# Kernel optimization log

Hardware: AMD Instinct MI355X
Metric: run time of the kernel (lower is better)

The kernel has to match this reference:

```python
import jax, jax.numpy as jnp
import numpy as np

LN_EPS = 1e-5

def _layernorm(x, g, b):
    mu = jnp.mean(x, axis=-1, keepdims=True)
    var = jnp.mean((x - mu) ** 2, axis=-1, keepdims=True)
    return (x - mu) * jax.lax.rsqrt(var + LN_EPS) * g + b

def _linear_init(k, fan_in, fan_out):
    s = 1.0 / np.sqrt(fan_in)
    kw, kb = jax.random.split(k)
    W = jax.random.uniform(kw, (fan_in, fan_out), jnp.float32, -s, s)
    b = jax.random.uniform(kb, (fan_out,), jnp.float32, -s, s)
    return W, b

def setup_inputs() -> dict:
    key = jax.random.key(0)
    ks = jax.random.split(key, 8)
    B, C, H, W = 4, 256, 64, 64
    Cout = 256
    N = H * W
    E = 16 * N
    x = jax.random.normal(ks[0], (B, C, H, W), jnp.float32)
    edge_index = jax.random.randint(ks[1], (2, E), 0, N)
    W1, b1 = _linear_init(ks[2], C, 1024)
    W2, b2 = _linear_init(ks[3], 1024, 512)
    W3, b3 = _linear_init(ks[4], 512, Cout)
    return {
        'x': x, 'edge_index': edge_index,
        'W1': W1, 'b1': b1, 'g1': jnp.ones(1024, jnp.float32), 'be1': jnp.zeros(1024, jnp.float32),
        'W2': W2, 'b2': b2, 'g2': jnp.ones(512, jnp.float32), 'be2': jnp.zeros(512, jnp.float32),
        'W3': W3, 'b3': b3, 'g_out': jnp.ones(Cout, jnp.float32), 'b_out': jnp.zeros(Cout, jnp.float32),
    }

def reference(x, edge_index, W1, b1, g1, be1, W2, b2, g2, be2, W3, b3, g_out, b_out):
    B, C, H, Wd = x.shape
    N = H * Wd
    # [B, N, C] node features (pixels as nodes)
    x_flat = x.reshape(B, C, N).transpose(0, 2, 1)
    # Dense adjacency from edge list (duplicates sum, same as sparse->to_dense).
    # Identical for every batch item, so build once and broadcast through einsum.
    A = jnp.zeros((N, N), x.dtype).at[edge_index[0], edge_index[1]].add(1.0)
    A = A + jnp.eye(N, dtype=x.dtype)  # self-loops
    deg = jnp.sum(A, axis=-1)
    d_inv_sqrt = jnp.where(deg > 0, jax.lax.rsqrt(deg), 0.0)
    A_norm = d_inv_sqrt[:, None] * A * d_inv_sqrt[None, :]
    # message passing: [N,N] @ [B,N,C] -> [B,N,C]
    h = jnp.einsum('mn,bnc->bmc', A_norm, x_flat)
    h = _layernorm(jax.nn.relu(h @ W1 + b1), g1, be1)
    h = _layernorm(jax.nn.relu(h @ W2 + b2), g2, be2)
    h = h @ W3 + b3
    h = _layernorm(h, g_out, b_out)
    return h.transpose(0, 2, 1).reshape(B, -1, H, Wd)
```

## Files before the change

kernel.cpp:

```cpp
#include <hip/hip_runtime.h>

typedef __attribute__((ext_vector_type(8))) short short8_t;
typedef __attribute__((ext_vector_type(4))) float f32x4;

#define AS1 __attribute__((address_space(1)))
#define AS3 __attribute__((address_space(3)))

static_assert(sizeof(short8_t) == 16, "short8_t must be 16B");

__device__ __forceinline__ short f2bf(float f) {
  union { float f; unsigned u; } v; v.f = f;
  unsigned r = (v.u + 0x7FFFu + ((v.u >> 16) & 1u)) >> 16;
  return (short)r;
}
__device__ __forceinline__ float bf2f(short s) {
  union { unsigned u; float f; } v; v.u = ((unsigned)(unsigned short)s) << 16;
  return v.f;
}

__global__ __launch_bounds__(256) void count_deg(const int* __restrict__ ei,
                                                 int* __restrict__ deg, int E) {
  int e = blockIdx.x * 256 + threadIdx.x;
  if (e < E) atomicAdd(&deg[ei[e]], 1);
}

__global__ __launch_bounds__(1024) void scan_deg(const int* __restrict__ deg,
                                                 int* __restrict__ rp,
                                                 float* __restrict__ dis) {
  __shared__ int part[1024];
  const int t = threadIdx.x;
  int4 v = ((const int4*)deg)[t];
  const int s = v.x + v.y + v.z + v.w;
  part[t] = s;
  __syncthreads();
  for (int off = 1; off < 1024; off <<= 1) {
    int mine = part[t];
    int add = (t >= off) ? part[t - off] : 0;
    __syncthreads();
    part[t] = mine + add;
    __syncthreads();
  }
  const int excl = part[t] - s;
  const int b4 = t * 4;
  rp[b4 + 0] = excl;
  rp[b4 + 1] = excl + v.x;
  rp[b4 + 2] = excl + v.x + v.y;
  rp[b4 + 3] = excl + v.x + v.y + v.z;
  if (t == 1023) rp[4096] = part[1023];
  dis[b4 + 0] = rsqrtf((float)(v.x + 1));
  dis[b4 + 1] = rsqrtf((float)(v.y + 1));
  dis[b4 + 2] = rsqrtf((float)(v.z + 1));
  dis[b4 + 3] = rsqrtf((float)(v.w + 1));
}

__global__ __launch_bounds__(256) void prep(
    const int* __restrict__ ei, const int* __restrict__ rp, int* __restrict__ fil,
    int* __restrict__ cols, int E,
    const float* __restrict__ x, const float* __restrict__ dis, short* __restrict__ xs,
    const float* __restrict__ W1, const float* __restrict__ W2, const float* __restrict__ W3,
    const float* __restrict__ g1, const float* __restrict__ be1,
    const float* __restrict__ g2, const float* __restrict__ be2,
    short* __restrict__ w1t, short* __restrict__ w2t, short* __restrict__ w3t,
    float* __restrict__ cs2, float* __restrict__ ct2,
    float* __restrict__ cs3, float* __restrict__ ct3) {
  __shared__ float tile[32][33];
  const int tx = threadIdx.x, ty = threadIdx.y;
  const int bid = blockIdx.x;
  if (bid < 256) {
    const int e = bid * 256 + ty * 32 + tx;
    if (e < E) {
      const int r = ei[e], c = ei[E + e];
      const int p = atomicAdd(&fil[r], 1);
      cols[rp[r] + p] = c;
    }
    return;
  }
  if (bid < 256 + 4096) {
    const int id = bid - 256;
    const int b = id >> 10;
    const int n0 = ((id & 1023) >> 3) * 32;
    const int c0 = (id & 7) * 32;
    const float* xb = x + (long)b * (256 * 4096);
#pragma unroll
    for (int i = 0; i < 32; i += 8)
      tile[ty + i][tx] = xb[(long)(c0 + ty + i) * 4096 + n0 + tx];
    __syncthreads();
#pragma unroll
    for (int i = 0; i < 32; i += 8) {
      const int n = n0 + ty + i;
      xs[(long)n * 1024 + b * 256 + c0 + tx] = f2bf(tile[tx][ty + i] * dis[n]);
    }
    return;
  }
  int id = bid - 4352;
  const float *Wf, *g = nullptr, *be = nullptr;
  float *cs = nullptr, *ctp = nullptr;
  short* Wt;
  int K, N, k0, n0;
  if (id < 256)      { Wf = W1; Wt = w1t; K = 256;  N = 1024; k0 = (id & 7) * 32;  n0 = (id >> 3) * 32; }
  else if (id < 768) { id -= 256; Wf = W2; Wt = w2t; K = 1024; N = 512; k0 = (id & 31) * 32; n0 = (id >> 5) * 32;
                       g = g1; be = be1; cs = cs2; ctp = ct2; }
  else               { id -= 768; Wf = W3; Wt = w3t; K = 512;  N = 256; k0 = (id & 15) * 32; n0 = (id >> 4) * 32;
                       g = g2; be = be2; cs = cs3; ctp = ct3; }
  float csp = 0.f, ctv = 0.f;
#pragma unroll
  for (int i = 0; i < 32; i += 8) {
    const int k = k0 + ty + i;
    const float wv = Wf[(long)k * N + n0 + tx];
    const float gk = g ? g[k] : 1.0f;
    tile[ty + i][tx] = gk * wv;
    csp += gk * wv;
    if (be) ctv += be[k] * wv;
  }
  __syncthreads();
#pragma unroll
  for (int i = 0; i < 32; i += 8)
    Wt[(long)(n0 + ty + i) * K + k0 + tx] = f2bf(tile[tx][ty + i]);
  if (cs) {
    atomicAdd(&cs[n0 + tx], csp);
    atomicAdd(&ctp[n0 + tx], ctv);
  }
}

__global__ __launch_bounds__(256) void gather_mp(const short* __restrict__ xs,
                                                 const float* __restrict__ dis,
                                                 const int* __restrict__ rp,
                                                 const int* __restrict__ cols,
                                                 short* __restrict__ h0) {
  __shared__ int sc[256];
  const int m = blockIdx.x;
  const int t = threadIdx.x;
  short4 v0 = ((const short4*)(xs + (long)m * 1024))[t];
  float a0 = bf2f(v0.x), a1 = bf2f(v0.y), a2 = bf2f(v0.z), a3 = bf2f(v0.w);
  const int s = rp[m], e = rp[m + 1];
  for (int base = s; base < e; base += 256) {
    const int cnt = min(256, e - base);
    __syncthreads();
    if (t < cnt) sc[t] = cols[base + t];
    __syncthreads();
    for (int j = 0; j < cnt; ++j) {
      const int n = sc[j];
      short4 v = ((const short4*)(xs + (long)n * 1024))[t];
      a0 += bf2f(v.x); a1 += bf2f(v.y); a2 += bf2f(v.z); a3 += bf2f(v.w);
    }
  }
  const float d = dis[m];
  short4 o;
  o.x = f2bf(a0 * d); o.y = f2bf(a1 * d); o.z = f2bf(a2 * d); o.w = f2bf(a3 * d);
  const int b = t >> 6, c4 = t & 63;
  ((short4*)(h0 + (((long)b << 12) + m) * 256))[c4] = o;
}

template <bool LNIN, bool RELU>
__global__ __launch_bounds__(256, 2) void gemm_ln(
    const short* __restrict__ A, const short* __restrict__ Bt,
    const float* __restrict__ bias, const float* __restrict__ cs,
    const float* __restrict__ ct, const float* __restrict__ statsIn,
    float* __restrict__ statsOut, short* __restrict__ out,
    int M, int N, int K) {
  __shared__ __align__(16) short As[2][128 * 32];
  __shared__ __align__(16) short Bs[2][128 * 32];
  const int tid = threadIdx.x;
  const int lane = tid & 63;
  const int wave = tid >> 6;
  const int wm = wave >> 1, wn = wave & 1;
  const int m0 = blockIdx.x * 128, n0 = blockIdx.y * 128;

  f32x4 acc[4][4] = {};

  const int srow = wave * 32 + (lane >> 2);
  const int scol = (lane & 3) * 8;
  const short* ag = A + (long)(m0 + srow) * K + scol;
  const short* bg = Bt + (long)(n0 + srow) * K + scol;
  const int ldst = (wave * 32) * 32;
  const int fr = lane & 15;
  const int kc = (lane >> 4) * 8;
  const int NT = K >> 5;

#define STAGE(T, BUF)                                                                        \
  do {                                                                                       \
    const short* a_ = ag + (T) * 32;                                                         \
    const short* b_ = bg + (T) * 32;                                                         \
    __builtin_amdgcn_global_load_lds((const AS1 void*)a_, (AS3 void*)(&As[BUF][ldst]), 16, 0, 0); \
    __builtin_amdgcn_global_load_lds((const AS1 void*)(a_ + 16 * K), (AS3 void*)(&As[BUF][ldst + 512]), 16, 0, 0); \
    __builtin_amdgcn_global_load_lds((const AS1 void*)b_, (AS3 void*)(&Bs[BUF][ldst]), 16, 0, 0); \
    __builtin_amdgcn_global_load_lds((const AS1 void*)(b_ + 16 * K), (AS3 void*)(&Bs[BUF][ldst + 512]), 16, 0, 0); \
  } while (0)

  STAGE(0, 0);
  __syncthreads();
  int cur = 0;
  for (int t = 0; t < NT; ++t) {
    if (t + 1 < NT) STAGE(t + 1, cur ^ 1);
    short8_t af[4], bf[4];
#pragma unroll
    for (int i = 0; i < 4; ++i)
      af[i] = *(const short8_t*)&As[cur][(wm * 64 + i * 16 + fr) * 32 + kc];
#pragma unroll
    for (int i = 0; i < 4; ++i)
      bf[i] = *(const short8_t*)&Bs[cur][(wn * 64 + i * 16 + fr) * 32 + kc];
#pragma unroll
    for (int mi = 0; mi < 4; ++mi)
#pragma unroll
      for (int ni = 0; ni < 4; ++ni)
        acc[mi][ni] = __builtin_amdgcn_mfma_f32_16x16x32_bf16(af[mi], bf[ni],
                                                              acc[mi][ni], 0, 0, 0);
    __syncthreads();
    cur ^= 1;
  }
#undef STAGE

  const int rq = (lane >> 4) * 4;
  const float invK = 1.0f / (float)K;
  float bv[4], csv[4], ctv[4];
#pragma unroll
  for (int ni = 0; ni < 4; ++ni) {
    const int col = n0 + wn * 64 + ni * 16 + fr;
    bv[ni] = bias[col];
    if (LNIN) { csv[ni] = cs[col]; ctv[ni] = ct[col]; }
  }
#pragma unroll
  for (int mi = 0; mi < 4; ++mi) {
    float r1[4], rmu[4];
    if (LNIN) {
#pragma unroll
      for (int r = 0; r < 4; ++r) {
        const int row = m0 + wm * 64 + mi * 16 + rq + r;
        const float s = statsIn[row * 2];
        const float q = statsIn[row * 2 + 1];
        const float mu = s * invK;
        const float var = fmaxf(q * invK - mu * mu, 0.0f);
        const float rr = rsqrtf(var + 1e-5f);
        r1[r] = rr; rmu[r] = rr * mu;
      }
    }
    float sv[4] = {0, 0, 0, 0}, qv[4] = {0, 0, 0, 0};
#pragma unroll
    for (int ni = 0; ni < 4; ++ni) {
      const int col = n0 + wn * 64 + ni * 16 + fr;
#pragma unroll
      for (int r = 0; r < 4; ++r) {
        const int row = m0 + wm * 64 + mi * 16 + rq + r;
        float v = acc[mi][ni][r];
        if (LNIN) v = r1[r] * v - rmu[r] * csv[ni] + ctv[ni] + bv[ni];
        else      v = v + bv[ni];
        if (RELU) v = fmaxf(v, 0.0f);
        out[(long)row * N + col] = f2bf(v);
        sv[r] += v; qv[r] += v * v;
      }
    }
#pragma unroll
    for (int r = 0; r < 4; ++r) {
      float s = sv[r], q = qv[r];
#pragma unroll
      for (int off = 1; off < 16; off <<= 1) {
        s += __shfl_xor(s, off);
        q += __shfl_xor(q, off);
      }
      if (fr == 0) {
        const int row = m0 + wm * 64 + mi * 16 + rq + r;
        atomicAdd(&statsOut[row * 2], s);
        atomicAdd(&statsOut[row * 2 + 1], q);
      }
    }
  }
}

__global__ __launch_bounds__(256) void ln_tr_out(const short* __restrict__ t3,
                                                 const float* __restrict__ stats,
                                                 const float* __restrict__ g,
                                                 const float* __restrict__ be,
                                                 float* __restrict__ out) {
  __shared__ short tile[64][66];
  const int tx = threadIdx.x;
  const int ty = threadIdx.y;
  const int n0 = blockIdx.x * 64;
  const int c0 = blockIdx.y * 64;
  const int b = blockIdx.z;
  const long rbase = ((long)b << 12) + n0;
#pragma unroll
  for (int i = ty; i < 64; i += 4)
    tile[i][tx] = t3[(rbase + i) * 256 + c0 + tx];
  const float s = stats[(rbase + tx) * 2];
  const float q = stats[(rbase + tx) * 2 + 1];
  const float mu = s * (1.0f / 256.0f);
  const float var = fmaxf(q * (1.0f / 256.0f) - mu * mu, 0.0f);
  const float inv = rsqrtf(var + 1e-5f);
  __syncthreads();
  float* ob = out + ((long)b << 20) + n0 + tx;
#pragma unroll
  for (int i = ty; i < 64; i += 4) {
    const int c = c0 + i;
    ob[(long)c * 4096] = (bf2f(tile[tx][i]) - mu) * inv * g[c] + be[c];
  }
}

extern "C" void kernel_launch(void* const* d_in, const int* in_sizes, int n_in,
                              void* d_out, int out_size, void* d_ws, size_t ws_size,
                              hipStream_t stream) {
  (void)n_in; (void)out_size; (void)ws_size;
  const float* x   = (const float*)d_in[0];
  const int*   ei  = (const int*)d_in[1];
  const float* W1  = (const float*)d_in[2];
  const float* b1  = (const float*)d_in[3];
  const float* g1  = (const float*)d_in[4];
  const float* be1 = (const float*)d_in[5];
  const float* W2  = (const float*)d_in[6];
  const float* b2  = (const float*)d_in[7];
  const float* g2  = (const float*)d_in[8];
  const float* be2 = (const float*)d_in[9];
  const float* W3  = (const float*)d_in[10];
  const float* b3  = (const float*)d_in[11];
  const float* go  = (const float*)d_in[12];
  const float* bo  = (const float*)d_in[13];
  float* out = (float*)d_out;
  const int E = in_sizes[1] / 2;

  char* w = (char*)d_ws;
  int*   deg    = (int*)(w + 0);
  int*   fil    = (int*)(w + (16 << 10));
  float* stats1 = (float*)(w + (32 << 10));
  float* stats2 = (float*)(w + (160 << 10));
  float* stats3 = (float*)(w + (288 << 10));
  float* cs2    = (float*)(w + (416 << 10));
  float* ct2    = (float*)(w + (418 << 10));
  float* cs3    = (float*)(w + (420 << 10));
  float* ct3    = (float*)(w + (421 << 10));
  int*   rp   = (int*)(w + (424 << 10));
  float* dis  = (float*)(w + (444 << 10));
  int*   cols = (int*)(w + (460 << 10));
  short* w1t  = (short*)(w + (720 << 10));
  short* w2t  = (short*)(w + (1240 << 10));
  short* w3t  = (short*)(w + (2264 << 10));
  short* xs   = (short*)(w + (3ull << 20));
  short* h0   = (short*)(w + (11ull << 20));
  short* t1   = (short*)(w + (19ull << 20));
  short* t2   = (short*)(w + (51ull << 20));
  short* t3   = (short*)(w + (67ull << 20));

  hipMemsetAsync(d_ws, 0, 422 << 10, stream);
  count_deg<<<256, 256, 0, stream>>>(ei, deg, E);
  scan_deg<<<1, 1024, 0, stream>>>(deg, rp, dis);
  prep<<<5248, dim3(32, 8), 0, stream>>>(ei, rp, fil, cols, E, x, dis, xs,
                                         W1, W2, W3, g1, be1, g2, be2,
                                         w1t, w2t, w3t, cs2, ct2, cs3, ct3);
  gather_mp<<<4096, 256, 0, stream>>>(xs, dis, rp, cols, h0);
  gemm_ln<false, true><<<dim3(128, 8), 256, 0, stream>>>(
      h0, w1t, b1, nullptr, nullptr, nullptr, stats1, t1, 16384, 1024, 256);
  gemm_ln<true, true><<<dim3(128, 4), 256, 0, stream>>>(
      t1, w2t, b2, cs2, ct2, stats1, stats2, t2, 16384, 512, 1024);
  gemm_ln<true, false><<<dim3(128, 2), 256, 0, stream>>>(
      t2, w3t, b3, cs3, ct3, stats2, stats3, t3, 16384, 256, 512);
  ln_tr_out<<<dim3(64, 4, 4), dim3(64, 4), 0, stream>>>(t3, stats3, go, bo, out);
}
```

Before: 147.7 us.

## Triple-buffer GEMM LDS pipeline and unroll gather loop by four

```diff
diff --git a/kernel.cpp b/kernel.cpp
--- a/kernel.cpp
+++ b/kernel.cpp
@@ -138,7 +138,19 @@
     __syncthreads();
     if (t < cnt) sc[t] = cols[base + t];
     __syncthreads();
-    for (int j = 0; j < cnt; ++j) {
+    int j = 0;
+    for (; j + 4 <= cnt; j += 4) {
+      const int n0 = sc[j], n1 = sc[j + 1], n2 = sc[j + 2], n3 = sc[j + 3];
+      short4 w0 = ((const short4*)(xs + (long)n0 * 1024))[t];
+      short4 w1 = ((const short4*)(xs + (long)n1 * 1024))[t];
+      short4 w2 = ((const short4*)(xs + (long)n2 * 1024))[t];
+      short4 w3 = ((const short4*)(xs + (long)n3 * 1024))[t];
+      a0 += bf2f(w0.x) + bf2f(w1.x) + bf2f(w2.x) + bf2f(w3.x);
+      a1 += bf2f(w0.y) + bf2f(w1.y) + bf2f(w2.y) + bf2f(w3.y);
+      a2 += bf2f(w0.z) + bf2f(w1.z) + bf2f(w2.z) + bf2f(w3.z);
+      a3 += bf2f(w0.w) + bf2f(w1.w) + bf2f(w2.w) + bf2f(w3.w);
+    }
+    for (; j < cnt; ++j) {
       const int n = sc[j];
       short4 v = ((const short4*)(xs + (long)n * 1024))[t];
       a0 += bf2f(v.x); a1 += bf2f(v.y); a2 += bf2f(v.z); a3 += bf2f(v.w);
@@ -158,8 +170,8 @@
     const float* __restrict__ ct, const float* __restrict__ statsIn,
     float* __restrict__ statsOut, short* __restrict__ out,
     int M, int N, int K) {
-  __shared__ __align__(16) short As[2][128 * 32];
-  __shared__ __align__(16) short Bs[2][128 * 32];
+  __shared__ __align__(16) short As[3][128 * 32];
+  __shared__ __align__(16) short Bs[3][128 * 32];
   const int tid = threadIdx.x;
   const int lane = tid & 63;
   const int wave = tid >> 6;
@@ -187,28 +199,41 @@
     __builtin_amdgcn_global_load_lds((const AS1 void*)(b_ + 16 * K), (AS3 void*)(&Bs[BUF][ldst + 512]), 16, 0, 0); \
   } while (0)
 
+#define COMPUTE(RB)                                                                          \
+  do {                                                                                       \
+    short8_t af[4], bf[4];                                                                   \
+    _Pragma("unroll")                                                                        \
+    for (int i = 0; i < 4; ++i)                                                              \
+      af[i] = *(const short8_t*)&As[RB][(wm * 64 + i * 16 + fr) * 32 + kc];                  \
+    _Pragma("unroll")                                                                        \
+    for (int i = 0; i < 4; ++i)                                                              \
+      bf[i] = *(const short8_t*)&Bs[RB][(wn * 64 + i * 16 + fr) * 32 + kc];                  \
+    _Pragma("unroll")                                                                        \
+    for (int mi = 0; mi < 4; ++mi)                                                           \
+      _Pragma("unroll")                                                                      \
+      for (int ni = 0; ni < 4; ++ni)                                                         \
+        acc[mi][ni] = __builtin_amdgcn_mfma_f32_16x16x32_bf16(af[mi], bf[ni],                \
+                                                              acc[mi][ni], 0, 0, 0);         \
+  } while (0)
+
   STAGE(0, 0);
-  __syncthreads();
-  int cur = 0;
-  for (int t = 0; t < NT; ++t) {
-    if (t + 1 < NT) STAGE(t + 1, cur ^ 1);
-    short8_t af[4], bf[4];
-#pragma unroll
-    for (int i = 0; i < 4; ++i)
-      af[i] = *(const short8_t*)&As[cur][(wm * 64 + i * 16 + fr) * 32 + kc];
-#pragma unroll
-    for (int i = 0; i < 4; ++i)
-      bf[i] = *(const short8_t*)&Bs[cur][(wn * 64 + i * 16 + fr) * 32 + kc];
-#pragma unroll
-    for (int mi = 0; mi < 4; ++mi)
-#pragma unroll
-      for (int ni = 0; ni < 4; ++ni)
-        acc[mi][ni] = __builtin_amdgcn_mfma_f32_16x16x32_bf16(af[mi], bf[ni],
-                                                              acc[mi][ni], 0, 0, 0);
-    __syncthreads();
-    cur ^= 1;
-  }
+  STAGE(1, 1);
+  int rb = 0;
+  for (int t = 0; t < NT - 1; ++t) {
+    asm volatile("s_waitcnt vmcnt(4)" ::: "memory");
+    __builtin_amdgcn_s_barrier();
+    __builtin_amdgcn_sched_barrier(0);
+    int wb = rb + 2; if (wb >= 3) wb -= 3;
+    if (t + 2 < NT) STAGE(t + 2, wb);
+    COMPUTE(rb);
+    rb = (rb == 2) ? 0 : rb + 1;
+  }
+  asm volatile("s_waitcnt vmcnt(0)" ::: "memory");
+  __builtin_amdgcn_s_barrier();
+  __builtin_amdgcn_sched_barrier(0);
+  COMPUTE(rb);
 #undef STAGE
+#undef COMPUTE
 
   const int rq = (lane >> 4) * 4;
   const float invK = 1.0f / (float)K;
```

After: 148.8 us. About the same (+0.7%).
